# Performance work log

Hardware: AMD Instinct MI355X
Metric: run time of the kernel (lower is better)

## Reference

```python
import jax, jax.numpy as jnp
import numpy as np

N_NODES = 100000
N_EDGES = 1250000
IN_DIM = 128
HID_DIM = 64
OUT_DIM = 16


def setup_inputs() -> dict:
    key = jax.random.key(0)
    k1, k2, k3, k4, k5, k6, k7 = jax.random.split(key, 7)
    x = jax.random.normal(k1, (N_NODES, IN_DIM), dtype=jnp.float32)
    edge_index = jax.random.randint(k2, (2, N_EDGES), 0, N_NODES, dtype=jnp.int64)
    s = 1.0 / np.sqrt(IN_DIM)
    W1 = jax.random.uniform(k3, (IN_DIM, HID_DIM), jnp.float32, -s, s)
    b1 = jax.random.uniform(k4, (HID_DIM,), jnp.float32, -s, s)
    s2 = 1.0 / np.sqrt(HID_DIM)
    W2 = jax.random.uniform(k5, (HID_DIM, OUT_DIM), jnp.float32, -s2, s2)
    b2 = jax.random.uniform(k6, (OUT_DIM,), jnp.float32, -s2, s2)
    return {"x": x, "edge_index": edge_index, "W1": W1, "b1": b1, "W2": W2, "b2": b2}


def reference(x, edge_index, W1, b1, W2, b2):
    # GCNConv (PyG default): linear transform, add self-loops, symmetric norm,
    # gather-scatter aggregation, bias. Then relu -> linear -> log_softmax.
    N = x.shape[0]
    loop = jnp.arange(N, dtype=edge_index.dtype)
    src = jnp.concatenate([edge_index[0], loop])  # message sources
    dst = jnpp_concat = jnp.concatenate([edge_index[1], loop])  # message targets
    # degree (with self-loops) computed on destination nodes
    deg = jax.ops.segment_sum(jnp.ones_like(dst, dtype=x.dtype), dst, num_segments=N)
    deg_inv_sqrt = jnp.where(deg > 0, jax.lax.rsqrt(deg), 0.0)
    norm = deg_inv_sqrt[src] * deg_inv_sqrt[dst]  # [E+N]
    h = x @ W1  # [N, hid] -- transform before aggregation (fewer bytes moved)
    msg = h[src] * norm[:, None]  # gather: [E+N, hid]
    agg = jax.ops.segment_sum(msg, dst, num_segments=N) + b1  # scatter-add
    h = jax.nn.relu(agg)
    logits = h @ W2 + b2
    return jax.nn.log_softmax(logits, axis=-1)
```

## Files before the change

kernel.cpp:

```cpp
#include <hip/hip_runtime.h>
#include <hip/hip_bf16.h>

#define N_NODES 100000
#define N_EDGES 1250000
#define IN_DIM  128
#define HID     64
#define OUTD    16
#define ROW     64
#define NRANGE  8
#define RSIZE   12500
#define NCHUNK  128
#define CHUNK   9768
#define FILLB   (NRANGE * NCHUNK)
#define MTILE   128
#define GEMMB   ((N_NODES + MTILE - 1) / MTILE)

typedef __attribute__((ext_vector_type(8))) short  short8;
typedef __attribute__((ext_vector_type(4))) float  floatx4;

__device__ __forceinline__ unsigned short f2bf(float f) {
    unsigned u = __float_as_uint(f);
    u += 0x7fffu + ((u >> 16) & 1u);
    return (unsigned short)(u >> 16);
}
__device__ __forceinline__ unsigned pk2(float lo, float hi) {
    __hip_bfloat162 t = __float22bfloat162_rn(make_float2(lo, hi));
    return *reinterpret_cast<unsigned*>(&t);
}
__device__ __forceinline__ float bf2f_lo(unsigned u) { return __uint_as_float(u << 16); }
__device__ __forceinline__ float bf2f_hi(unsigned u) { return __uint_as_float(u & 0xffff0000u); }

__global__ __launch_bounds__(256) void zero_cursor(int* __restrict__ cursor,
                                                   unsigned* __restrict__ hb_dummy) {
    int i = blockIdx.x * 256 + threadIdx.x;
    if (i < N_NODES) cursor[i] = 0;
    if (i < 32) hb_dummy[i] = 0u;
}

__global__ __launch_bounds__(256) void fill_gemm(const float* __restrict__ x,
                                                 const float* __restrict__ W1,
                                                 const int* __restrict__ src,
                                                 const int* __restrict__ dst,
                                                 int* __restrict__ cursor,
                                                 int* __restrict__ csr,
                                                 unsigned short* __restrict__ hb) {
    __shared__ unsigned short w1t[HID][132];

    if (blockIdx.x < FILLB) {
        const int r  = blockIdx.x & 7;
        const int c  = blockIdx.x >> 3;
        const int lo = r * RSIZE;
        const int q1 = min(N_EDGES, (c + 1) * CHUNK) >> 2;
        for (int q = (c * CHUNK >> 2) + threadIdx.x; q < q1; q += 256) {
            int4 d4 = ((const int4*)dst)[q];
            int  e  = q << 2;
#pragma unroll
            for (int u = 0; u < 4; u++) {
                int d = (u == 0) ? d4.x : (u == 1) ? d4.y : (u == 2) ? d4.z : d4.w;
                if ((unsigned)(d - lo) < (unsigned)RSIZE) {
                    int s = src[e + u];
                    int p = atomicAdd(&cursor[d], 1);
                    if (p < ROW) csr[(size_t)d * ROW + p] = s;
                }
            }
        }
        return;
    }

    const int m0 = (blockIdx.x - FILLB) * MTILE;

    for (int q = threadIdx.x; q < IN_DIM * HID / 4; q += 256) {
        int k = q >> 4, n = (q & 15) * 4;
        float4 wq = ((const float4*)W1)[q];
        w1t[n + 0][k] = f2bf(wq.x);
        w1t[n + 1][k] = f2bf(wq.y);
        w1t[n + 2][k] = f2bf(wq.z);
        w1t[n + 3][k] = f2bf(wq.w);
    }
    __syncthreads();

    const int lane = threadIdx.x & 63;
    const int w    = threadIdx.x >> 6;
    const int mrow = lane & 15;
    const int quad = lane >> 4;
    const int rowa = min(m0 + w * 32 + mrow,      N_NODES - 1);
    const int rowb = min(m0 + w * 32 + 16 + mrow, N_NODES - 1);

    floatx4 acc[2][4] = {};
#pragma unroll
    for (int k0 = 0; k0 < IN_DIM; k0 += 32) {
        union { unsigned u[4]; short8 s; } a0, a1;
        {
            const float4* pa = (const float4*)(x + (size_t)rowa * IN_DIM + k0 + quad * 8);
            float4 u0 = pa[0], v0 = pa[1];
            a0.u[0] = pk2(u0.x, u0.y); a0.u[1] = pk2(u0.z, u0.w);
            a0.u[2] = pk2(v0.x, v0.y); a0.u[3] = pk2(v0.z, v0.w);
            const float4* pb = (const float4*)(x + (size_t)rowb * IN_DIM + k0 + quad * 8);
            float4 u1 = pb[0], v1 = pb[1];
            a1.u[0] = pk2(u1.x, u1.y); a1.u[1] = pk2(u1.z, u1.w);
            a1.u[2] = pk2(v1.x, v1.y); a1.u[3] = pk2(v1.z, v1.w);
        }
        short8 b0 = *(const short8*)&w1t[ 0 + mrow][k0 + quad * 8];
        short8 b1 = *(const short8*)&w1t[16 + mrow][k0 + quad * 8];
        short8 b2 = *(const short8*)&w1t[32 + mrow][k0 + quad * 8];
        short8 b3 = *(const short8*)&w1t[48 + mrow][k0 + quad * 8];
        acc[0][0] = __builtin_amdgcn_mfma_f32_16x16x32_bf16(a0.s, b0, acc[0][0], 0, 0, 0);
        acc[0][1] = __builtin_amdgcn_mfma_f32_16x16x32_bf16(a0.s, b1, acc[0][1], 0, 0, 0);
        acc[0][2] = __builtin_amdgcn_mfma_f32_16x16x32_bf16(a0.s, b2, acc[0][2], 0, 0, 0);
        acc[0][3] = __builtin_amdgcn_mfma_f32_16x16x32_bf16(a0.s, b3, acc[0][3], 0, 0, 0);
        acc[1][0] = __builtin_amdgcn_mfma_f32_16x16x32_bf16(a1.s, b0, acc[1][0], 0, 0, 0);
        acc[1][1] = __builtin_amdgcn_mfma_f32_16x16x32_bf16(a1.s, b1, acc[1][1], 0, 0, 0);
        acc[1][2] = __builtin_amdgcn_mfma_f32_16x16x32_bf16(a1.s, b2, acc[1][2], 0, 0, 0);
        acc[1][3] = __builtin_amdgcn_mfma_f32_16x16x32_bf16(a1.s, b3, acc[1][3], 0, 0, 0);
    }

#pragma unroll
    for (int tm = 0; tm < 2; tm++) {
#pragma unroll
        for (int reg = 0; reg < 4; reg++) {
            int m = m0 + w * 32 + tm * 16 + quad * 4 + reg;
            if (m < N_NODES) {
#pragma unroll
                for (int tn = 0; tn < 4; tn++)
                    hb[(size_t)m * HID + tn * 16 + mrow] = f2bf(acc[tm][tn][reg]);
            }
        }
    }
}

__global__ __launch_bounds__(256) void scale_kernel(const int* __restrict__ cursor,
                                                    float* __restrict__ dis,
                                                    unsigned short* __restrict__ hb) {
    int gid = blockIdx.x * 256 + threadIdx.x;
    if (gid >= N_NODES * (HID / 4)) return;
    int i = gid >> 4;
    float di = rsqrtf((float)cursor[i] + 1.0f);
    if ((gid & 15) == 0) dis[i] = di;
    uint2* p = (uint2*)hb + gid;
    uint2 v = *p;
    *p = make_uint2(pk2(bf2f_lo(v.x) * di, bf2f_hi(v.x) * di),
                    pk2(bf2f_lo(v.y) * di, bf2f_hi(v.y) * di));
}

__global__ __launch_bounds__(256) void pull_epilogue(const unsigned short* __restrict__ hb,
                                                     const int* __restrict__ csr,
                                                     const int* __restrict__ deg,
                                                     const float* __restrict__ dis,
                                                     const float* __restrict__ b1,
                                                     const float* __restrict__ W2,
                                                     const float* __restrict__ b2,
                                                     float* __restrict__ out) {
    const int i     = blockIdx.x * 4 + (threadIdx.x >> 6);
    const int lane  = threadIdx.x & 63;
    const int e_sub = lane >> 4;
    const int f4    = lane & 15;

    const int   cnt = min(deg[i], ROW);
    const float di  = dis[i];

    int s_l = N_NODES;
    if (lane < cnt) s_l = csr[(size_t)i * ROW + lane];

    uint2 hs = ((const uint2*)(hb + (size_t)i * HID))[f4];

    float ax = 0.f, ay = 0.f, az = 0.f, aw = 0.f;
    const int G = (cnt + 3) >> 2;
    int g = 0;
    for (; g + 2 <= G; g += 2) {
        int e0 = (g << 2) + e_sub, e1 = e0 + 4;
        int s0 = __shfl(s_l, e0, 64), s1 = __shfl(s_l, e1, 64);
        uint2 a = ((const uint2*)(hb + (size_t)s0 * HID))[f4];
        uint2 b = ((const uint2*)(hb + (size_t)s1 * HID))[f4];
        ax += bf2f_lo(a.x); ay += bf2f_hi(a.x); az += bf2f_lo(a.y); aw += bf2f_hi(a.y);
        ax += bf2f_lo(b.x); ay += bf2f_hi(b.x); az += bf2f_lo(b.y); aw += bf2f_hi(b.y);
    }
    if (g < G) {
        int e0 = (g << 2) + e_sub;
        int s0 = __shfl(s_l, e0, 64);
        uint2 a = ((const uint2*)(hb + (size_t)s0 * HID))[f4];
        ax += bf2f_lo(a.x); ay += bf2f_hi(a.x); az += bf2f_lo(a.y); aw += bf2f_hi(a.y);
    }

    ax += __shfl_xor(ax, 16, 64); ax += __shfl_xor(ax, 32, 64);
    ay += __shfl_xor(ay, 16, 64); ay += __shfl_xor(ay, 32, 64);
    az += __shfl_xor(az, 16, 64); az += __shfl_xor(az, 32, 64);
    aw += __shfl_xor(aw, 16, 64); aw += __shfl_xor(aw, 32, 64);

    float4 b1v = ((const float4*)b1)[f4];
    float v0 = fmaxf(fmaf(ax + bf2f_lo(hs.x), di, b1v.x), 0.f);
    float v1 = fmaxf(fmaf(ay + bf2f_hi(hs.x), di, b1v.y), 0.f);
    float v2 = fmaxf(fmaf(az + bf2f_lo(hs.y), di, b1v.z), 0.f);
    float v3 = fmaxf(fmaf(aw + bf2f_hi(hs.y), di, b1v.w), 0.f);

    const float4* W2v = (const float4*)W2;
    float4 w0 = W2v[(4 * f4 + 0) * 4 + e_sub];
    float4 w1 = W2v[(4 * f4 + 1) * 4 + e_sub];
    float4 w2 = W2v[(4 * f4 + 2) * 4 + e_sub];
    float4 w3 = W2v[(4 * f4 + 3) * 4 + e_sub];
    float p0 = v0 * w0.x + v1 * w1.x + v2 * w2.x + v3 * w3.x;
    float p1 = v0 * w0.y + v1 * w1.y + v2 * w2.y + v3 * w3.y;
    float p2 = v0 * w0.z + v1 * w1.z + v2 * w2.z + v3 * w3.z;
    float p3 = v0 * w0.w + v1 * w1.w + v2 * w2.w + v3 * w3.w;
#pragma unroll
    for (int d = 1; d < 16; d <<= 1) {
        p0 += __shfl_xor(p0, d, 64);
        p1 += __shfl_xor(p1, d, 64);
        p2 += __shfl_xor(p2, d, 64);
        p3 += __shfl_xor(p3, d, 64);
    }
    float4 b2v = ((const float4*)b2)[e_sub];
    float lg0 = p0 + b2v.x, lg1 = p1 + b2v.y, lg2 = p2 + b2v.z, lg3 = p3 + b2v.w;

    float m = fmaxf(fmaxf(lg0, lg1), fmaxf(lg2, lg3));
    m = fmaxf(m, __shfl_xor(m, 16, 64));
    m = fmaxf(m, __shfl_xor(m, 32, 64));
    float s = __expf(lg0 - m) + __expf(lg1 - m) + __expf(lg2 - m) + __expf(lg3 - m);
    s += __shfl_xor(s, 16, 64);
    s += __shfl_xor(s, 32, 64);
    float lse = __logf(s) + m;

    if (f4 == 0) {
        float4 o = make_float4(lg0 - lse, lg1 - lse, lg2 - lse, lg3 - lse);
        ((float4*)out)[(size_t)i * 4 + e_sub] = o;
    }
}

extern "C" void kernel_launch(void* const* d_in, const int* in_sizes, int n_in,
                              void* d_out, int out_size, void* d_ws, size_t ws_size,
                              hipStream_t stream) {
    const float* x   = (const float*)d_in[0];
    const int*   ei  = (const int*)d_in[1];
    const float* W1  = (const float*)d_in[2];
    const float* b1  = (const float*)d_in[3];
    const float* W2  = (const float*)d_in[4];
    const float* b2  = (const float*)d_in[5];
    float*       out = (float*)d_out;

    const int* src = ei;
    const int* dst = ei + N_EDGES;

    char* ws = (char*)d_ws;
    size_t off = 0;
    unsigned short* hb = (unsigned short*)(ws + off);
    off += (size_t)(N_NODES + 1) * HID * 2;
    int*   csr    = (int*)  (ws + off); off += ((size_t)N_NODES * ROW + ROW) * 4;
    int*   cursor = (int*)  (ws + off); off += (size_t)N_NODES * 4;
    float* dis    = (float*)(ws + off); off += (size_t)N_NODES * 4;

    zero_cursor<<<(N_NODES + 255) / 256, 256, 0, stream>>>(
        cursor, (unsigned*)(hb + (size_t)N_NODES * HID));
    fill_gemm<<<FILLB + GEMMB, 256, 0, stream>>>(x, W1, src, dst, cursor, csr, hb);
    scale_kernel<<<(N_NODES * (HID / 4) + 255) / 256, 256, 0, stream>>>(cursor, dis, hb);
    pull_epilogue<<<N_NODES / 4, 256, 0, stream>>>(hb, csr, cursor, dis, b1, W2, b2, out);
}
```

Measured before the change: 237.1 us.

## Split fill from GEMM, fuse degree scaling into GEMM epilogue, widen gather loads

The combined fill+GEMM kernel is split into two kernels. The GEMM now runs after the degree counts are final, so it applies the rsqrt degree scale in its epilogue and writes dis, which removes the separate scale_kernel pass over hb. The fill grid is doubled to 256 chunks per range. The pull kernel now uses 8 lanes per edge with 16-byte loads and folds the self-loop into the neighbor list by capping at 63 entries. The cost is that fill and GEMM no longer overlap inside one launch.

```diff
diff --git a/kernel.cpp b/kernel.cpp
--- a/kernel.cpp
+++ b/kernel.cpp
@@ -9,8 +9,8 @@
 #define ROW     64
 #define NRANGE  8
 #define RSIZE   12500
-#define NCHUNK  128
-#define CHUNK   9768
+#define NCHUNK  256
+#define CHUNK   4888
 #define FILLB   (NRANGE * NCHUNK)
 #define MTILE   128
 #define GEMMB   ((N_NODES + MTILE - 1) / MTILE)
@@ -37,37 +37,37 @@
     if (i < 32) hb_dummy[i] = 0u;
 }
 
-__global__ __launch_bounds__(256) void fill_gemm(const float* __restrict__ x,
+__global__ __launch_bounds__(256) void fill_kernel(const int* __restrict__ src,
+                                                   const int* __restrict__ dst,
+                                                   int* __restrict__ cursor,
+                                                   int* __restrict__ csr) {
+    const int r  = blockIdx.x & 7;
+    const int c  = blockIdx.x >> 3;
+    const int lo = r * RSIZE;
+    const int q1 = min(N_EDGES, (c + 1) * CHUNK) >> 2;
+    for (int q = (c * CHUNK >> 2) + threadIdx.x; q < q1; q += 256) {
+        int4 d4 = ((const int4*)dst)[q];
+        int  e  = q << 2;
+#pragma unroll
+        for (int u = 0; u < 4; u++) {
+            int d = (u == 0) ? d4.x : (u == 1) ? d4.y : (u == 2) ? d4.z : d4.w;
+            if ((unsigned)(d - lo) < (unsigned)RSIZE) {
+                int s = src[e + u];
+                int p = atomicAdd(&cursor[d], 1);
+                if (p < ROW) csr[(size_t)d * ROW + p] = s;
+            }
+        }
+    }
+}
+
+__global__ __launch_bounds__(256) void gemm_mfma(const float* __restrict__ x,
                                                  const float* __restrict__ W1,
-                                                 const int* __restrict__ src,
-                                                 const int* __restrict__ dst,
-                                                 int* __restrict__ cursor,
-                                                 int* __restrict__ csr,
+                                                 const int* __restrict__ cursor,
+                                                 float* __restrict__ dis,
                                                  unsigned short* __restrict__ hb) {
     __shared__ unsigned short w1t[HID][132];
 
-    if (blockIdx.x < FILLB) {
-        const int r  = blockIdx.x & 7;
-        const int c  = blockIdx.x >> 3;
-        const int lo = r * RSIZE;
-        const int q1 = min(N_EDGES, (c + 1) * CHUNK) >> 2;
-        for (int q = (c * CHUNK >> 2) + threadIdx.x; q < q1; q += 256) {
-            int4 d4 = ((const int4*)dst)[q];
-            int  e  = q << 2;
-#pragma unroll
-            for (int u = 0; u < 4; u++) {
-                int d = (u == 0) ? d4.x : (u == 1) ? d4.y : (u == 2) ? d4.z : d4.w;
-                if ((unsigned)(d - lo) < (unsigned)RSIZE) {
-                    int s = src[e + u];
-                    int p = atomicAdd(&cursor[d], 1);
-                    if (p < ROW) csr[(size_t)d * ROW + p] = s;
-                }
-            }
-        }
-        return;
-    }
-
-    const int m0 = (blockIdx.x - FILLB) * MTILE;
+    const int m0 = blockIdx.x * MTILE;
 
     for (int q = threadIdx.x; q < IN_DIM * HID / 4; q += 256) {
         int k = q >> 4, n = (q & 15) * 4;
@@ -120,26 +120,17 @@
         for (int reg = 0; reg < 4; reg++) {
             int m = m0 + w * 32 + tm * 16 + quad * 4 + reg;
             if (m < N_NODES) {
+                float di = rsqrtf((float)cursor[m] + 1.0f);
 #pragma unroll
                 for (int tn = 0; tn < 4; tn++)
-                    hb[(size_t)m * HID + tn * 16 + mrow] = f2bf(acc[tm][tn][reg]);
+                    hb[(size_t)m * HID + tn * 16 + mrow] = f2bf(acc[tm][tn][reg] * di);
             }
         }
     }
-}
-
-__global__ __launch_bounds__(256) void scale_kernel(const int* __restrict__ cursor,
-                                                    float* __restrict__ dis,
-                                                    unsigned short* __restrict__ hb) {
-    int gid = blockIdx.x * 256 + threadIdx.x;
-    if (gid >= N_NODES * (HID / 4)) return;
-    int i = gid >> 4;
-    float di = rsqrtf((float)cursor[i] + 1.0f);
-    if ((gid & 15) == 0) dis[i] = di;
-    uint2* p = (uint2*)hb + gid;
-    uint2 v = *p;
-    *p = make_uint2(pk2(bf2f_lo(v.x) * di, bf2f_hi(v.x) * di),
-                    pk2(bf2f_lo(v.y) * di, bf2f_hi(v.y) * di));
+    if (threadIdx.x < MTILE) {
+        int m = m0 + threadIdx.x;
+        if (m < N_NODES) dis[m] = rsqrtf((float)cursor[m] + 1.0f);
+    }
 }
 
 __global__ __launch_bounds__(256) void pull_epilogue(const unsigned short* __restrict__ hb,
@@ -150,79 +141,91 @@
                                                      const float* __restrict__ W2,
                                                      const float* __restrict__ b2,
                                                      float* __restrict__ out) {
-    const int i     = blockIdx.x * 4 + (threadIdx.x >> 6);
-    const int lane  = threadIdx.x & 63;
-    const int e_sub = lane >> 4;
-    const int f4    = lane & 15;
-
-    const int   cnt = min(deg[i], ROW);
+    const int i    = blockIdx.x * 4 + (threadIdx.x >> 6);
+    const int lane = threadIdx.x & 63;
+    const int e8   = lane >> 3;
+    const int f8   = lane & 7;
+
+    const int   cnt = min(deg[i], 63);
     const float di  = dis[i];
 
     int s_l = N_NODES;
     if (lane < cnt) s_l = csr[(size_t)i * ROW + lane];
-
-    uint2 hs = ((const uint2*)(hb + (size_t)i * HID))[f4];
-
-    float ax = 0.f, ay = 0.f, az = 0.f, aw = 0.f;
-    const int G = (cnt + 3) >> 2;
+    if (lane == cnt) s_l = i;
+
+    float a0 = 0.f, a1 = 0.f, a2 = 0.f, a3 = 0.f,
+          a4 = 0.f, a5 = 0.f, a6 = 0.f, a7 = 0.f;
+    const int G = (cnt + 1 + 7) >> 3;
     int g = 0;
     for (; g + 2 <= G; g += 2) {
-        int e0 = (g << 2) + e_sub, e1 = e0 + 4;
-        int s0 = __shfl(s_l, e0, 64), s1 = __shfl(s_l, e1, 64);
-        uint2 a = ((const uint2*)(hb + (size_t)s0 * HID))[f4];
-        uint2 b = ((const uint2*)(hb + (size_t)s1 * HID))[f4];
-        ax += bf2f_lo(a.x); ay += bf2f_hi(a.x); az += bf2f_lo(a.y); aw += bf2f_hi(a.y);
-        ax += bf2f_lo(b.x); ay += bf2f_hi(b.x); az += bf2f_lo(b.y); aw += bf2f_hi(b.y);
+        int sA = __shfl(s_l, (g << 3) + e8, 64);
+        int sB = __shfl(s_l, ((g + 1) << 3) + e8, 64);
+        uint4 hA = ((const uint4*)(hb + (size_t)sA * HID))[f8];
+        uint4 hB = ((const uint4*)(hb + (size_t)sB * HID))[f8];
+        a0 += bf2f_lo(hA.x); a1 += bf2f_hi(hA.x);
+        a2 += bf2f_lo(hA.y); a3 += bf2f_hi(hA.y);
+        a4 += bf2f_lo(hA.z); a5 += bf2f_hi(hA.z);
+        a6 += bf2f_lo(hA.w); a7 += bf2f_hi(hA.w);
+        a0 += bf2f_lo(hB.x); a1 += bf2f_hi(hB.x);
+        a2 += bf2f_lo(hB.y); a3 += bf2f_hi(hB.y);
+        a4 += bf2f_lo(hB.z); a5 += bf2f_hi(hB.z);
+        a6 += bf2f_lo(hB.w); a7 += bf2f_hi(hB.w);
     }
     if (g < G) {
-        int e0 = (g << 2) + e_sub;
-        int s0 = __shfl(s_l, e0, 64);
-        uint2 a = ((const uint2*)(hb + (size_t)s0 * HID))[f4];
-        ax += bf2f_lo(a.x); ay += bf2f_hi(a.x); az += bf2f_lo(a.y); aw += bf2f_hi(a.y);
-    }
-
-    ax += __shfl_xor(ax, 16, 64); ax += __shfl_xor(ax, 32, 64);
-    ay += __shfl_xor(ay, 16, 64); ay += __shfl_xor(ay, 32, 64);
-    az += __shfl_xor(az, 16, 64); az += __shfl_xor(az, 32, 64);
-    aw += __shfl_xor(aw, 16, 64); aw += __shfl_xor(aw, 32, 64);
-
-    float4 b1v = ((const float4*)b1)[f4];
-    float v0 = fmaxf(fmaf(ax + bf2f_lo(hs.x), di, b1v.x), 0.f);
-    float v1 = fmaxf(fmaf(ay + bf2f_hi(hs.x), di, b1v.y), 0.f);
-    float v2 = fmaxf(fmaf(az + bf2f_lo(hs.y), di, b1v.z), 0.f);
-    float v3 = fmaxf(fmaf(aw + bf2f_hi(hs.y), di, b1v.w), 0.f);
-
-    const float4* W2v = (const float4*)W2;
-    float4 w0 = W2v[(4 * f4 + 0) * 4 + e_sub];
-    float4 w1 = W2v[(4 * f4 + 1) * 4 + e_sub];
-    float4 w2 = W2v[(4 * f4 + 2) * 4 + e_sub];
-    float4 w3 = W2v[(4 * f4 + 3) * 4 + e_sub];
-    float p0 = v0 * w0.x + v1 * w1.x + v2 * w2.x + v3 * w3.x;
-    float p1 = v0 * w0.y + v1 * w1.y + v2 * w2.y + v3 * w3.y;
-    float p2 = v0 * w0.z + v1 * w1.z + v2 * w2.z + v3 * w3.z;
-    float p3 = v0 * w0.w + v1 * w1.w + v2 * w2.w + v3 * w3.w;
-#pragma unroll
-    for (int d = 1; d < 16; d <<= 1) {
+        int sA = __shfl(s_l, (g << 3) + e8, 64);
+        uint4 hA = ((const uint4*)(hb + (size_t)sA * HID))[f8];
+        a0 += bf2f_lo(hA.x); a1 += bf2f_hi(hA.x);
+        a2 += bf2f_lo(hA.y); a3 += bf2f_hi(hA.y);
+        a4 += bf2f_lo(hA.z); a5 += bf2f_hi(hA.z);
+        a6 += bf2f_lo(hA.w); a7 += bf2f_hi(hA.w);
+    }
+
+#pragma unroll
+    for (int d = 8; d < 64; d <<= 1) {
+        a0 += __shfl_xor(a0, d, 64); a1 += __shfl_xor(a1, d, 64);
+        a2 += __shfl_xor(a2, d, 64); a3 += __shfl_xor(a3, d, 64);
+        a4 += __shfl_xor(a4, d, 64); a5 += __shfl_xor(a5, d, 64);
+        a6 += __shfl_xor(a6, d, 64); a7 += __shfl_xor(a7, d, 64);
+    }
+
+    float4 bA = ((const float4*)b1)[f8 * 2];
+    float4 bB = ((const float4*)b1)[f8 * 2 + 1];
+    float v0 = fmaxf(fmaf(a0, di, bA.x), 0.f);
+    float v1 = fmaxf(fmaf(a1, di, bA.y), 0.f);
+    float v2 = fmaxf(fmaf(a2, di, bA.z), 0.f);
+    float v3 = fmaxf(fmaf(a3, di, bA.w), 0.f);
+    float v4 = fmaxf(fmaf(a4, di, bB.x), 0.f);
+    float v5 = fmaxf(fmaf(a5, di, bB.y), 0.f);
+    float v6 = fmaxf(fmaf(a6, di, bB.z), 0.f);
+    float v7 = fmaxf(fmaf(a7, di, bB.w), 0.f);
+
+    const float2* W2v = (const float2*)W2;
+    float p0 = 0.f, p1 = 0.f;
+    float vv[8] = {v0, v1, v2, v3, v4, v5, v6, v7};
+#pragma unroll
+    for (int j = 0; j < 8; j++) {
+        float2 w = W2v[(f8 * 8 + j) * 8 + e8];
+        p0 = fmaf(vv[j], w.x, p0);
+        p1 = fmaf(vv[j], w.y, p1);
+    }
+#pragma unroll
+    for (int d = 1; d < 8; d <<= 1) {
         p0 += __shfl_xor(p0, d, 64);
         p1 += __shfl_xor(p1, d, 64);
-        p2 += __shfl_xor(p2, d, 64);
-        p3 += __shfl_xor(p3, d, 64);
-    }
-    float4 b2v = ((const float4*)b2)[e_sub];
-    float lg0 = p0 + b2v.x, lg1 = p1 + b2v.y, lg2 = p2 + b2v.z, lg3 = p3 + b2v.w;
-
-    float m = fmaxf(fmaxf(lg0, lg1), fmaxf(lg2, lg3));
-    m = fmaxf(m, __shfl_xor(m, 16, 64));
-    m = fmaxf(m, __shfl_xor(m, 32, 64));
-    float s = __expf(lg0 - m) + __expf(lg1 - m) + __expf(lg2 - m) + __expf(lg3 - m);
-    s += __shfl_xor(s, 16, 64);
-    s += __shfl_xor(s, 32, 64);
+    }
+    float2 b2v = ((const float2*)b2)[e8];
+    float lg0 = p0 + b2v.x, lg1 = p1 + b2v.y;
+
+    float m = fmaxf(lg0, lg1);
+#pragma unroll
+    for (int d = 8; d < 64; d <<= 1) m = fmaxf(m, __shfl_xor(m, d, 64));
+    float s = __expf(lg0 - m) + __expf(lg1 - m);
+#pragma unroll
+    for (int d = 8; d < 64; d <<= 1) s += __shfl_xor(s, d, 64);
     float lse = __logf(s) + m;
 
-    if (f4 == 0) {
-        float4 o = make_float4(lg0 - lse, lg1 - lse, lg2 - lse, lg3 - lse);
-        ((float4*)out)[(size_t)i * 4 + e_sub] = o;
-    }
+    if (f8 == 0)
+        ((float2*)out)[(size_t)i * 8 + e8] = make_float2(lg0 - lse, lg1 - lse);
 }
 
 extern "C" void kernel_launch(void* const* d_in, const int* in_sizes, int n_in,
@@ -249,7 +252,7 @@
 
     zero_cursor<<<(N_NODES + 255) / 256, 256, 0, stream>>>(
         cursor, (unsigned*)(hb + (size_t)N_NODES * HID));
-    fill_gemm<<<FILLB + GEMMB, 256, 0, stream>>>(x, W1, src, dst, cursor, csr, hb);
-    scale_kernel<<<(N_NODES * (HID / 4) + 255) / 256, 256, 0, stream>>>(cursor, dis, hb);
+    fill_kernel<<<FILLB, 256, 0, stream>>>(src, dst, cursor, csr);
+    gemm_mfma<<<GEMMB, 256, 0, stream>>>(x, W1, cursor, dis, hb);
     pull_epilogue<<<N_NODES / 4, 256, 0, stream>>>(hb, csr, cursor, dis, b1, W2, b2, out);
 }
```

Result: slower. 269.1 us (+13.5%).
